# Kernel tuning notes

Measured on AMD Instinct MI355X. Metric: run time of the kernel, lower is better.

The kernel has to match this reference:

```python
import jax, jax.numpy as jnp
import numpy as np

N_ENT, N_REL, N_TS, RANK, BATCH = 400000, 500, 365, 64, 256


def complex_mul(e1, e2):
    a, b = jnp.split(e1, 2, axis=1)
    c, d = jnp.split(e2, 2, axis=1)
    return jnp.concatenate([a * c + b * d, a * d - b * c], axis=1)


def quaternion_mul(e1, e2):
    a, b, c, d = jnp.split(e1, 4, axis=1)
    e, f, g, h = jnp.split(e2, 4, axis=1)
    return jnp.concatenate([
        a * e - b * f - c * g - d * h,
        b * e + a * f + c * h - d * g,
        c * e + a * g + d * f - b * h,
        d * e + a * h + b * g - c * f,
    ], axis=1)


def setup_inputs() -> dict:
    key = jax.random.key(0)
    k0, k1, k2, k3, k4, kx = jax.random.split(key, 6)
    s = 0.05  # xavier-ish scale
    E0 = jax.random.normal(k0, (N_ENT, RANK), dtype=jnp.float32) * s
    E1 = jax.random.normal(k1, (N_REL, RANK), dtype=jnp.float32) * s
    E2 = jax.random.normal(k2, (N_TS, RANK), dtype=jnp.float32) * s
    E3 = jax.random.normal(k3, (N_TS, RANK), dtype=jnp.float32) * s
    E4 = jax.random.normal(k4, (N_TS, RANK), dtype=jnp.float32) * s
    x = jax.random.randint(kx, (BATCH, 4), 0, N_TS, dtype=jnp.int64)
    return {"E0": E0, "E1": E1, "E2": E2, "E3": E3, "E4": E4, "x": x}


def reference(E0, E1, E2, E3, E4, x):
    # Training mode, disable_path=True, disable_cl=True
    lhs = E0[x[:, 0]]          # [B, R]
    rel = E1[x[:, 1]]          # [B, R]
    time_ent = E2[x[:, 3]]     # [B, R]
    time_rel = E3[x[:, 3]]     # [B, R]
    comp_time = E4[x[:, 3]]    # [B, R]

    rel_ = rel + complex_mul(rel, comp_time)
    neis_embd = jnp.zeros_like(lhs)  # path encoder disabled

    lhs_rel = quaternion_mul(
        jnp.concatenate([lhs, lhs, time_ent, time_ent], axis=1),
        jnp.concatenate([rel_, rel_, time_rel, time_rel], axis=1),
    )
    a, b, c, d = jnp.split(lhs_rel, 4, axis=1)  # each [B, R]

    # a@all_en + b@all_en fused as (a+b)@E0^T; per-row scalar terms broadcast
    row_bias = (jnp.sum(c * neis_embd, axis=1)
                + jnp.sum(d * time_ent, axis=1)
                + jnp.sum(d * neis_embd, axis=1)
                + jnp.sum(c * time_ent, axis=1))
    scores = (a + b) @ E0.T + row_bias[:, None]  # [B, N_ENT]

    cl_loss = jnp.zeros((), dtype=scores.dtype)
    return scores, cl_loss, (E2[:-1], E3[:-1], E4[:-1])
```

## Files before the change

kernel.cpp:

```cpp
#include <hip/hip_runtime.h>

#define N_ENT 400000
#define N_REL 500
#define N_TS 365
#define RANK 64
#define BATCH 256

typedef __attribute__((ext_vector_type(8))) __bf16 bf16x8;
typedef __attribute__((ext_vector_type(16))) float f32x16;
typedef __attribute__((ext_vector_type(4))) float f32x4;

__global__ void prep_tail_kernel(const float* __restrict__ E0,
                                 const float* __restrict__ E1,
                                 const float* __restrict__ E2,
                                 const float* __restrict__ E3,
                                 const float* __restrict__ E4,
                                 const int* __restrict__ x,
                                 __bf16* __restrict__ Vbf,
                                 float* __restrict__ bias,
                                 float* __restrict__ out)
{
    const int b = blockIdx.x;
    const int k = threadIdx.x;

    const long long SCORES = (long long)BATCH * N_ENT;
    const int CP = (N_TS - 1) * RANK;

    if (b == 364 && k == 0) out[SCORES] = 0.0f;
    if (b < N_TS - 1) {
        const int idx = b * RANK + k;
        out[SCORES + 1 + 0LL * CP + idx] = E2[idx];
        out[SCORES + 1 + 1LL * CP + idx] = E3[idx];
        out[SCORES + 1 + 2LL * CP + idx] = E4[idx];
    }

    if (b < BATCH) {
        const int i = b;
        const int i0 = x[i * 4 + 0];
        const int i1 = x[i * 4 + 1];
        const int i3 = x[i * 4 + 3];

        const float lhs = E0[i0 * RANK + k];
        const float rel = E1[i1 * RANK + k];
        const float te  = E2[i3 * RANK + k];
        const float tr  = E3[i3 * RANK + k];

        const int  kh = k & 31;
        const float a = E1[i1 * RANK + kh];
        const float bb = E1[i1 * RANK + 32 + kh];
        const float c = E4[i3 * RANK + kh];
        const float d = E4[i3 * RANK + 32 + kh];
        const float cm = (k < 32) ? (a * c + bb * d) : (a * d - bb * c);
        const float rel_ = rel + cm;

        const float v = 2.0f * (lhs * rel_ - te * tr);
        Vbf[i * RANK + k] = (__bf16)v;

        float rb = 2.0f * te * (lhs * tr + te * rel_);
        #pragma unroll
        for (int off = 32; off > 0; off >>= 1)
            rb += __shfl_down(rb, off, 64);
        if (k == 0) bias[i] = rb;
    }
}

__global__ __launch_bounds__(256) void scores_mfma(
    const float* __restrict__ E0,
    const __bf16* __restrict__ Vbf,
    const float* __restrict__ bias,
    float* __restrict__ out)
{
    __shared__ float tile[2][32][128];
    __shared__ float sbias[BATCH];

    const int t    = threadIdx.x;
    const int lane = t & 63;
    const int wid  = t >> 6;
    const int l31  = lane & 31;
    const int h    = lane >> 5;
    const int colbase = blockIdx.x * 128;
    const int col  = colbase + wid * 32 + l31;
    const int khalf = h * 8;

    sbias[t] = bias[t];

    bf16x8 bfrag[4];
    const float* erow = E0 + (size_t)col * RANK;
    #pragma unroll
    for (int f = 0; f < 4; ++f) {
        const int kb = f * 16 + khalf;
        const float4 u0 = *reinterpret_cast<const float4*>(erow + kb);
        const float4 u1 = *reinterpret_cast<const float4*>(erow + kb + 4);
        bfrag[f][0] = (__bf16)u0.x;  bfrag[f][1] = (__bf16)u0.y;
        bfrag[f][2] = (__bf16)u0.z;  bfrag[f][3] = (__bf16)u0.w;
        bfrag[f][4] = (__bf16)u1.x;  bfrag[f][5] = (__bf16)u1.y;
        bfrag[f][6] = (__bf16)u1.z;  bfrag[f][7] = (__bf16)u1.w;
    }

    int p = 0;
    #pragma unroll 1
    for (int mt = 0; mt < 8; ++mt) {
        const __bf16* arow = Vbf + (size_t)(mt * 32 + l31) * RANK + khalf;

        f32x16 acc;
        #pragma unroll
        for (int j = 0; j < 16; ++j) acc[j] = 0.0f;

        #pragma unroll
        for (int f = 0; f < 4; ++f) {
            const bf16x8 afrag = *reinterpret_cast<const bf16x8*>(arow + f * 16);
            acc = __builtin_amdgcn_mfma_f32_32x32x16_bf16(afrag, bfrag[f], acc, 0, 0, 0);
        }

        #pragma unroll
        for (int j = 0; j < 16; ++j) {
            const int row = (j & 3) + 8 * (j >> 2) + 4 * h;
            tile[p][row][wid * 32 + l31] = acc[j];
        }
        __syncthreads();

        const int m0 = mt * 32;
        #pragma unroll
        for (int q = 0; q < 4; ++q) {
            const int row = q * 8 + (t >> 5);
            f32x4 v = *reinterpret_cast<const f32x4*>(&tile[p][row][(t & 31) * 4]);
            const float bv = sbias[m0 + row];
            v.x += bv; v.y += bv; v.z += bv; v.w += bv;
            *reinterpret_cast<f32x4*>(
                &out[(size_t)(m0 + row) * N_ENT + colbase + (t & 31) * 4]) = v;
        }
        p ^= 1;
    }
}

extern "C" void kernel_launch(void* const* d_in, const int* in_sizes, int n_in,
                              void* d_out, int out_size, void* d_ws, size_t ws_size,
                              hipStream_t stream) {
    const float* E0 = (const float*)d_in[0];
    const float* E1 = (const float*)d_in[1];
    const float* E2 = (const float*)d_in[2];
    const float* E3 = (const float*)d_in[3];
    const float* E4 = (const float*)d_in[4];
    const int*   x  = (const int*)d_in[5];

    float* out = (float*)d_out;

    float*  bias = (float*)d_ws;
    __bf16* Vbf  = (__bf16*)((char*)d_ws + 1024);

    prep_tail_kernel<<<N_TS, RANK, 0, stream>>>(E0, E1, E2, E3, E4, x, Vbf, bias, out);

    const int nblk = N_ENT / 128;
    scores_mfma<<<nblk, 256, 0, stream>>>(E0, Vbf, bias, out);
}
```

Measured before the change: 120.0 us.

## Use per-wave padded LDS tiles to drop block barriers and prefetch A fragments

The epilogue now stages each wave's 32x32 accumulator tile in its own padded LDS region and writes it out within that same wave. This removes the block-wide __syncthreads on every M-tile iteration, and the padding is meant to cut LDS bank conflicts. The Vbf A-fragments for the next M-tile are loaded before the current tile's epilogue, so global load latency overlaps the store phase. The trade-off is that each wave now stores 128-byte row segments instead of 512-byte segments per block row, and every wave redundantly loads the full bias vector.

```diff
diff --git a/kernel.cpp b/kernel.cpp
--- a/kernel.cpp
+++ b/kernel.cpp
@@ -70,8 +70,8 @@
     const float* __restrict__ bias,
     float* __restrict__ out)
 {
-    __shared__ float tile[2][32][128];
-    __shared__ float sbias[BATCH];
+    __shared__ __align__(16) float lt[4][32][36];
+    __shared__ float sb[BATCH];
 
     const int t    = threadIdx.x;
     const int lane = t & 63;
@@ -79,10 +79,13 @@
     const int l31  = lane & 31;
     const int h    = lane >> 5;
     const int colbase = blockIdx.x * 128;
-    const int col  = colbase + wid * 32 + l31;
+    const int wcol = colbase + wid * 32;
+    const int col  = wcol + l31;
     const int khalf = h * 8;
 
-    sbias[t] = bias[t];
+    #pragma unroll
+    for (int r = 0; r < 4; ++r)
+        sb[r * 64 + lane] = bias[r * 64 + lane];
 
     bf16x8 bfrag[4];
     const float* erow = E0 + (size_t)col * RANK;
@@ -97,39 +100,51 @@
         bfrag[f][6] = (__bf16)u1.z;  bfrag[f][7] = (__bf16)u1.w;
     }
 
-    int p = 0;
+    float (*tile)[36] = lt[wid];
+    const int rrow = lane >> 3;
+    const int rcol = (lane & 7) * 4;
+
+    const __bf16* abase = Vbf + (size_t)l31 * RANK + khalf;
+
+    bf16x8 a0 = *reinterpret_cast<const bf16x8*>(abase);
+    bf16x8 a1 = *reinterpret_cast<const bf16x8*>(abase + 16);
+    bf16x8 a2 = *reinterpret_cast<const bf16x8*>(abase + 32);
+    bf16x8 a3 = *reinterpret_cast<const bf16x8*>(abase + 48);
+
     #pragma unroll 1
     for (int mt = 0; mt < 8; ++mt) {
-        const __bf16* arow = Vbf + (size_t)(mt * 32 + l31) * RANK + khalf;
-
         f32x16 acc;
         #pragma unroll
         for (int j = 0; j < 16; ++j) acc[j] = 0.0f;
+        acc = __builtin_amdgcn_mfma_f32_32x32x16_bf16(a0, bfrag[0], acc, 0, 0, 0);
+        acc = __builtin_amdgcn_mfma_f32_32x32x16_bf16(a1, bfrag[1], acc, 0, 0, 0);
+        acc = __builtin_amdgcn_mfma_f32_32x32x16_bf16(a2, bfrag[2], acc, 0, 0, 0);
+        acc = __builtin_amdgcn_mfma_f32_32x32x16_bf16(a3, bfrag[3], acc, 0, 0, 0);
 
-        #pragma unroll
-        for (int f = 0; f < 4; ++f) {
-            const bf16x8 afrag = *reinterpret_cast<const bf16x8*>(arow + f * 16);
-            acc = __builtin_amdgcn_mfma_f32_32x32x16_bf16(afrag, bfrag[f], acc, 0, 0, 0);
-        }
+        const __bf16* anext = abase + (size_t)(((mt + 1) & 7) * 32) * RANK;
+        const bf16x8 n0 = *reinterpret_cast<const bf16x8*>(anext);
+        const bf16x8 n1 = *reinterpret_cast<const bf16x8*>(anext + 16);
+        const bf16x8 n2 = *reinterpret_cast<const bf16x8*>(anext + 32);
+        const bf16x8 n3 = *reinterpret_cast<const bf16x8*>(anext + 48);
 
         #pragma unroll
         for (int j = 0; j < 16; ++j) {
             const int row = (j & 3) + 8 * (j >> 2) + 4 * h;
-            tile[p][row][wid * 32 + l31] = acc[j];
+            tile[row][l31] = acc[j];
         }
-        __syncthreads();
 
         const int m0 = mt * 32;
         #pragma unroll
         for (int q = 0; q < 4; ++q) {
-            const int row = q * 8 + (t >> 5);
-            f32x4 v = *reinterpret_cast<const f32x4*>(&tile[p][row][(t & 31) * 4]);
-            const float bv = sbias[m0 + row];
+            const int row = q * 8 + rrow;
+            const int m = m0 + row;
+            f32x4 v = *reinterpret_cast<const f32x4*>(&tile[row][rcol]);
+            const float bv = sb[m];
             v.x += bv; v.y += bv; v.z += bv; v.w += bv;
-            *reinterpret_cast<f32x4*>(
-                &out[(size_t)(m0 + row) * N_ENT + colbase + (t & 31) * 4]) = v;
+            *reinterpret_cast<f32x4*>(&out[(size_t)m * N_ENT + wcol + rcol]) = v;
         }
-        p ^= 1;
+
+        a0 = n0; a1 = n1; a2 = n2; a3 = n3;
     }
 }
 
```

Measured after the change: 134.5 us. 12.1% more time.

## Widen scores tile to 256 columns with XCD-aware block swizzle

Applied to the files above, without the earlier changes.

Each block now computes 256 entity columns instead of 128, so the A fragments loaded per batch tile feed two MFMA chains. Block indices are remapped so that consecutive column ranges land on the same XCD, aiming for better L2 locality. The store phase writes full 1KB row segments per wave, which gives wider contiguous writes. In exchange the double-buffered tile is replaced by a single buffer with an extra barrier per iteration, the grid is halved, and tail columns need guards.

```diff
diff --git a/kernel.cpp b/kernel.cpp
--- a/kernel.cpp
+++ b/kernel.cpp
@@ -70,66 +70,85 @@
     const float* __restrict__ bias,
     float* __restrict__ out)
 {
-    __shared__ float tile[2][32][128];
-    __shared__ float sbias[BATCH];
+    __shared__ __align__(16) float tile[32][256];
+    __shared__ float sb[BATCH];
 
     const int t    = threadIdx.x;
     const int lane = t & 63;
     const int wid  = t >> 6;
     const int l31  = lane & 31;
     const int h    = lane >> 5;
-    const int colbase = blockIdx.x * 128;
-    const int col  = colbase + wid * 32 + l31;
     const int khalf = h * 8;
 
-    sbias[t] = bias[t];
+    const int nwg = gridDim.x;
+    const int qq  = nwg >> 3;
+    const int rr  = nwg & 7;
+    const int xcd = blockIdx.x & 7;
+    const int idx = blockIdx.x >> 3;
+    const int swz = (xcd < rr ? xcd * (qq + 1) : rr * (qq + 1) + (xcd - rr) * qq) + idx;
 
-    bf16x8 bfrag[4];
-    const float* erow = E0 + (size_t)col * RANK;
+    const int colbase = swz * 256;
+    const bool has_c1 = (colbase + 128) < N_ENT;
+
+    sb[t] = bias[t];
+
+    bf16x8 bfrag[2][4];
     #pragma unroll
-    for (int f = 0; f < 4; ++f) {
-        const int kb = f * 16 + khalf;
-        const float4 u0 = *reinterpret_cast<const float4*>(erow + kb);
-        const float4 u1 = *reinterpret_cast<const float4*>(erow + kb + 4);
-        bfrag[f][0] = (__bf16)u0.x;  bfrag[f][1] = (__bf16)u0.y;
-        bfrag[f][2] = (__bf16)u0.z;  bfrag[f][3] = (__bf16)u0.w;
-        bfrag[f][4] = (__bf16)u1.x;  bfrag[f][5] = (__bf16)u1.y;
-        bfrag[f][6] = (__bf16)u1.z;  bfrag[f][7] = (__bf16)u1.w;
+    for (int c = 0; c < 2; ++c) {
+        if (c == 1 && !has_c1) break;
+        const float* erow = E0 + (size_t)(colbase + c * 128 + wid * 32 + l31) * RANK;
+        #pragma unroll
+        for (int f = 0; f < 4; ++f) {
+            const int kb = f * 16 + khalf;
+            const float4 u0 = *reinterpret_cast<const float4*>(erow + kb);
+            const float4 u1 = *reinterpret_cast<const float4*>(erow + kb + 4);
+            bfrag[c][f][0] = (__bf16)u0.x;  bfrag[c][f][1] = (__bf16)u0.y;
+            bfrag[c][f][2] = (__bf16)u0.z;  bfrag[c][f][3] = (__bf16)u0.w;
+            bfrag[c][f][4] = (__bf16)u1.x;  bfrag[c][f][5] = (__bf16)u1.y;
+            bfrag[c][f][6] = (__bf16)u1.z;  bfrag[c][f][7] = (__bf16)u1.w;
+        }
     }
 
-    int p = 0;
     #pragma unroll 1
     for (int mt = 0; mt < 8; ++mt) {
         const __bf16* arow = Vbf + (size_t)(mt * 32 + l31) * RANK + khalf;
-
-        f32x16 acc;
+        bf16x8 afrag[4];
         #pragma unroll
-        for (int j = 0; j < 16; ++j) acc[j] = 0.0f;
+        for (int f = 0; f < 4; ++f)
+            afrag[f] = *reinterpret_cast<const bf16x8*>(arow + f * 16);
 
         #pragma unroll
-        for (int f = 0; f < 4; ++f) {
-            const bf16x8 afrag = *reinterpret_cast<const bf16x8*>(arow + f * 16);
-            acc = __builtin_amdgcn_mfma_f32_32x32x16_bf16(afrag, bfrag[f], acc, 0, 0, 0);
-        }
+        for (int c = 0; c < 2; ++c) {
+            if (c == 1 && !has_c1) break;
+            f32x16 acc;
+            #pragma unroll
+            for (int j = 0; j < 16; ++j) acc[j] = 0.0f;
+            #pragma unroll
+            for (int f = 0; f < 4; ++f)
+                acc = __builtin_amdgcn_mfma_f32_32x32x16_bf16(afrag[f], bfrag[c][f], acc, 0, 0, 0);
 
-        #pragma unroll
-        for (int j = 0; j < 16; ++j) {
-            const int row = (j & 3) + 8 * (j >> 2) + 4 * h;
-            tile[p][row][wid * 32 + l31] = acc[j];
+            #pragma unroll
+            for (int j = 0; j < 16; ++j) {
+                const int row = (j & 3) + 8 * (j >> 2) + 4 * h;
+                tile[row][c * 128 + wid * 32 + l31] = acc[j];
+            }
         }
         __syncthreads();
 
         const int m0 = mt * 32;
+        const int cd = lane * 4;
+        const bool sok = (colbase + cd) < N_ENT;
         #pragma unroll
-        for (int q = 0; q < 4; ++q) {
-            const int row = q * 8 + (t >> 5);
-            f32x4 v = *reinterpret_cast<const f32x4*>(&tile[p][row][(t & 31) * 4]);
-            const float bv = sbias[m0 + row];
+        for (int qp = 0; qp < 8; ++qp) {
+            const int row = qp * 4 + wid;
+            const int m = m0 + row;
+            f32x4 v = *reinterpret_cast<const f32x4*>(&tile[row][cd]);
+            const float bv = sb[m];
             v.x += bv; v.y += bv; v.z += bv; v.w += bv;
-            *reinterpret_cast<f32x4*>(
-                &out[(size_t)(m0 + row) * N_ENT + colbase + (t & 31) * 4]) = v;
+            if (sok)
+                *reinterpret_cast<f32x4*>(&out[(size_t)m * N_ENT + colbase + cd]) = v;
         }
-        p ^= 1;
+        __syncthreads();
     }
 }
 
@@ -150,6 +169,6 @@
 
     prep_tail_kernel<<<N_TS, RANK, 0, stream>>>(E0, E1, E2, E3, E4, x, Vbf, bias, out);
 
-    const int nblk = N_ENT / 128;
+    const int nblk = (N_ENT + 255) / 256;
     scores_mfma<<<nblk, 256, 0, stream>>>(E0, Vbf, bias, out);
 }
```

Measured after the change: 120.8 us. Within noise of the previous version (+0.7%).
